# Performance work log

Measured on AMD Instinct MI355X. Metric: run time of the kernel, lower is better.

The kernel has to match this reference:

```python
import math
import jax, jax.numpy as jnp
import numpy as np

NUM_HEADS = 12
NUM_GROUPS = 12
NUM_BUCKETS = 32
MAX_DISTANCE = 128
EPS_GN = 1e-5
EPS_LN = 1e-5


def _layernorm(x, w, b):
    mu = x.mean(axis=-1, keepdims=True)
    xc = x - mu
    inv = jax.lax.rsqrt((xc * xc).mean(axis=-1, keepdims=True) + EPS_LN)
    return xc * inv * w + b


def _rel_pos_bias(T, emb):
    # T5-style bucketed relative position bias -> (1, n_heads, T, T)
    ctx = jnp.arange(T)[:, None]
    mem = jnp.arange(T)[None, :]
    n = -(mem - ctx)  # = context - memory
    nb = NUM_BUCKETS // 2  # bidirectional
    ret = (n < 0).astype(jnp.int32) * nb
    n = jnp.abs(n)
    max_exact = nb // 2
    val_large = max_exact + (
        jnp.log(jnp.maximum(n, 1).astype(jnp.float32) / max_exact)
        / math.log(MAX_DISTANCE / max_exact) * (nb - max_exact)
    ).astype(jnp.int32)
    val_large = jnp.minimum(val_large, nb - 1)
    bucket = ret + jnp.where(n < max_exact, n, val_large)  # (T, T)
    vals = emb[bucket]  # (T, T, He)
    return jnp.transpose(vals, (2, 0, 1))[None]  # (1, He, T, T)


def setup_inputs() -> dict:
    key = jax.random.key(0)
    ks = jax.random.split(key, 12)
    T, B, C, H, W, D = 64, 1, 768, 8, 8, 8
    hd = C // NUM_HEADS
    return {
        "x": jax.random.normal(ks[0], (T, B, C, H, W, D), jnp.float32),
        "norm1_w": jax.random.normal(ks[1], (C,), jnp.float32),
        "w_in": jax.random.normal(ks[2], (3 * C, C), jnp.float32) * 0.02,
        "b_in": jax.random.normal(ks[3], (3 * C,), jnp.float32) * 0.02,
        "qn_w": jax.random.normal(ks[4], (hd,), jnp.float32),
        "qn_b": jnp.zeros((hd,), jnp.float32),
        "kn_w": jax.random.normal(ks[5], (hd,), jnp.float32),
        "kn_b": jnp.zeros((hd,), jnp.float32),
        "rel_emb": jax.random.normal(ks[6], (NUM_BUCKETS, NUM_HEADS), jnp.float32),
        "w_out": jax.random.normal(ks[7], (C, C), jnp.float32) * 0.02,
        "b_out": jax.random.normal(ks[8], (C,), jnp.float32) * 0.02,
        "gamma": jax.random.normal(ks[9], (C,), jnp.float32) * 1e-6,
    }


def reference(x, norm1_w, w_in, b_in, qn_w, qn_b, kn_w, kn_b, rel_emb, w_out, b_out, gamma):
    T, B, C, H, W, D = x.shape
    He = NUM_HEADS
    hd = C // He
    xt = x.reshape(T * B, C, H, W, D)

    # RMSGroupNorm (actually standard group_norm, weight only, no bias)
    xg = xt.reshape(T * B, NUM_GROUPS, C // NUM_GROUPS, H, W, D)
    mu = xg.mean(axis=(2, 3, 4, 5), keepdims=True)
    var = ((xg - mu) ** 2).mean(axis=(2, 3, 4, 5), keepdims=True)
    xn = (xg - mu) * jax.lax.rsqrt(var + EPS_GN)
    xn = xn.reshape(T * B, C, H, W, D) * norm1_w[None, :, None, None, None]

    # 1x1x1 Conv3d input head == per-voxel linear
    qkv = jnp.einsum('ncxyz,oc->noxyz', xn, w_in) + b_in[None, :, None, None, None]

    # rearrange '(t b) (he c) h w d -> (b h w d) he t c'
    qkv = qkv.reshape(T, B, He, 3 * hd, H, W, D)
    qkv = jnp.transpose(qkv, (1, 4, 5, 6, 2, 0, 3)).reshape(B * H * W * D, He, T, 3 * hd)
    q, k, v = jnp.split(qkv, 3, axis=-1)
    q = _layernorm(q, qn_w, qn_b)
    k = _layernorm(k, kn_w, kn_b)

    bias = _rel_pos_bias(T, rel_emb)  # (1, He, T, T)
    scores = jnp.einsum('nhtc,nhsc->nhts', q, k) / math.sqrt(hd) + bias
    att = jax.nn.softmax(scores, axis=-1)
    o = jnp.einsum('nhts,nhsc->nhtc', att, v)  # (BHWD, He, T, hd)

    # rearrange '(b h w d) he t c -> (t b) (he c) h w d'
    o = o.reshape(B, H, W, D, He, T, hd)
    o = jnp.transpose(o, (5, 0, 4, 6, 1, 2, 3)).reshape(T * B, C, H, W, D)

    o = jnp.einsum('ncxyz,oc->noxyz', o, w_out) + b_out[None, :, None, None, None]
    o = o.reshape(T, B, C, H, W, D)

    # layer-scale residual (drop_path = identity)
    return x + gamma[None, None, :, None, None, None] * o
```

## Files before the change

### kernel.cpp

```cpp
#include <hip/hip_runtime.h>


typedef unsigned int u32;
typedef unsigned short u16;
typedef __attribute__((ext_vector_type(4))) float f32x4;
typedef __attribute__((ext_vector_type(8))) short s16x8;

__device__ __forceinline__ float bfl(u32 w){ union{u32 i; float f;} u; u.i = w<<16; return u.f; }
__device__ __forceinline__ float bfh(u32 w){ union{u32 i; float f;} u; u.i = w & 0xffff0000u; return u.f; }
__device__ __forceinline__ u16 f2bf(float f){ union{float ff; u32 i;} u; u.ff = f; u32 r = u.i + 0x7fffu + ((u.i>>16)&1u); return (u16)(r>>16); }
__device__ __forceinline__ u32 pk2(float a, float b){ return (u32)f2bf(a) | ((u32)f2bf(b)<<16); }

__global__ void k_bias(const float* __restrict__ rel, float* __restrict__ bias_d){
  int d = threadIdx.x;
  if (d < 127){
    int delta = d - 63;
    int ret = (delta < 0) ? 16 : 0;
    int a = delta < 0 ? -delta : delta;
    int bkt;
    if (a < 8) bkt = a;
    else {
      float lr = (logf((float)a * 0.125f) / logf(16.0f)) * 8.0f;
      int vl = 8 + (int)lr;
      bkt = vl > 15 ? 15 : vl;
    }
    bkt += ret;
    for (int he = 0; he < 12; ++he) bias_d[he*128 + d] = rel[bkt*12 + he];
  }
}

__global__ void k_cast(const float* __restrict__ a, const float* __restrict__ b,
                       u16* __restrict__ ab, u16* __restrict__ bb){
  const int n1 = 2304*768, n2 = 768*768;
  for (int i = blockIdx.x*blockDim.x + threadIdx.x; i < n1+n2; i += gridDim.x*blockDim.x){
    if (i < n1) ab[i] = f2bf(a[i]);
    else        bb[i-n1] = f2bf(b[i-n1]);
  }
}

__global__ __launch_bounds__(256) void k_stats(const float* __restrict__ x, float* __restrict__ stats){
  __shared__ float red[8];
  const float4* xb = (const float4*)(x + (size_t)blockIdx.x * 32768);
  float s = 0.f, s2 = 0.f;
  for (int i = threadIdx.x; i < 8192; i += 256){
    float4 v = xb[i];
    s  += v.x + v.y + v.z + v.w;
    s2 += v.x*v.x + v.y*v.y + v.z*v.z + v.w*v.w;
  }
  #pragma unroll
  for (int off = 32; off; off >>= 1){ s += __shfl_down(s, off); s2 += __shfl_down(s2, off); }
  int wid = threadIdx.x >> 6;
  if ((threadIdx.x & 63) == 0){ red[wid*2] = s; red[wid*2+1] = s2; }
  __syncthreads();
  if (threadIdx.x == 0){
    float ts = 0.f, ts2 = 0.f;
    for (int w = 0; w < 4; ++w){ ts += red[w*2]; ts2 += red[w*2+1]; }
    float mu  = ts * (1.f/32768.f);
    float var = ts2 * (1.f/32768.f) - mu*mu;
    stats[blockIdx.x*2]   = mu;
    stats[blockIdx.x*2+1] = rsqrtf(var + 1e-5f);
  }
}

__global__ __launch_bounds__(256) void k_norm(const float* __restrict__ x, const float* __restrict__ stats,
                                              const float* __restrict__ w1, u16* __restrict__ xnT){
  __shared__ float ld[64][65];
  const int b = blockIdx.x;
  const int tb = b / 96, rem = b % 96, cb = rem >> 3, vb = rem & 7;
  const float mu  = stats[(tb*12+cb)*2];
  const float inv = stats[(tb*12+cb)*2+1];
  const int tid = threadIdx.x;
  #pragma unroll
  for (int it = 0; it < 4; ++it){
    int chunk = it*256 + tid;
    int cl = chunk >> 4, v4 = chunk & 15;
    float w = w1[cb*64 + cl] * inv;
    float4 v = *(const float4*)(x + ((size_t)(tb*768 + cb*64 + cl)*512 + vb*64 + v4*4));
    ld[cl][v4*4+0] = (v.x - mu) * w;
    ld[cl][v4*4+1] = (v.y - mu) * w;
    ld[cl][v4*4+2] = (v.z - mu) * w;
    ld[cl][v4*4+3] = (v.w - mu) * w;
  }
  __syncthreads();
  #pragma unroll
  for (int it = 0; it < 2; ++it){
    int chunk = it*256 + tid;
    int vl = chunk >> 3, p = chunk & 7;
    u32 ow[4];
    #pragma unroll
    for (int j = 0; j < 4; ++j)
      ow[j] = pk2(ld[p*8 + j*2][vl], ld[p*8 + j*2 + 1][vl]);
    uint4 q4; q4.x = ow[0]; q4.y = ow[1]; q4.z = ow[2]; q4.w = ow[3];
    *(uint4*)(xnT + ((size_t)(tb*512 + vb*64 + vl)*768 + cb*64 + p*8)) = q4;
  }
}

__global__ __launch_bounds__(256) void k_gemm(const u16* __restrict__ At, const u16* __restrict__ Bt,
    const int M, const int K, const int mtiles, const int epi,
    const float* __restrict__ bias, u16* __restrict__ outT,
    const float* __restrict__ xres, const float* __restrict__ gamma,
    const float* __restrict__ bout, float* __restrict__ outp)
{
  __shared__ u16 lta[128*32];
  __shared__ u16 ltb[128*32];
  const int tid = threadIdx.x;
  const int l = tid & 63;
  const int wid = tid >> 6;
  const int wm = wid & 1, wn = wid >> 1;
  const int mt = blockIdx.x % mtiles, nt = blockIdx.x / mtiles;
  const f32x4 z = {0.f, 0.f, 0.f, 0.f};
  f32x4 acc[4][4];
  #pragma unroll
  for (int i = 0; i < 4; ++i)
    #pragma unroll
    for (int j = 0; j < 4; ++j) acc[i][j] = z;
  const int nk = K >> 5;
  const int r0 = tid >> 2, q0 = tid & 3;
  for (int kt = 0; kt < nk; ++kt){
    uint4 av0 = *(const uint4*)(At + (size_t)(mt*128 + r0     )*K + kt*32 + q0*8);
    uint4 bv0 = *(const uint4*)(Bt + (size_t)(nt*128 + r0     )*K + kt*32 + q0*8);
    uint4 av1 = *(const uint4*)(At + (size_t)(mt*128 + r0 + 64)*K + kt*32 + q0*8);
    uint4 bv1 = *(const uint4*)(Bt + (size_t)(nt*128 + r0 + 64)*K + kt*32 + q0*8);
    __syncthreads();
    *(uint4*)&lta[(r0     )*32 + q0*8] = av0;
    *(uint4*)&ltb[(r0     )*32 + q0*8] = bv0;
    *(uint4*)&lta[(r0 + 64)*32 + q0*8] = av1;
    *(uint4*)&ltb[(r0 + 64)*32 + q0*8] = bv1;
    __syncthreads();
    s16x8 fa[4], fb[4];
    #pragma unroll
    for (int f = 0; f < 4; ++f){
      fa[f] = *(const s16x8*)&ltb[(wn*64 + f*16 + (l&15))*32 + ((l>>4)<<3)];
      fb[f] = *(const s16x8*)&lta[(wm*64 + f*16 + (l&15))*32 + ((l>>4)<<3)];
    }
    #pragma unroll
    for (int fn = 0; fn < 4; ++fn)
      #pragma unroll
      for (int fm = 0; fm < 4; ++fm)
        acc[fn][fm] = __builtin_amdgcn_mfma_f32_16x16x32_bf16(fa[fn], fb[fm], acc[fn][fm], 0, 0, 0);
  }
  const int rsub = (l>>4) << 2, cbase = l & 15;
  if (epi == 1){
    #pragma unroll
    for (int fn = 0; fn < 4; ++fn)
      #pragma unroll
      for (int fm = 0; fm < 4; ++fm){
        const int n0 = nt*128 + wn*64 + fn*16 + rsub;
        const int m  = mt*128 + wm*64 + fm*16 + cbase;
        const float bm = bias[m];
        #pragma unroll
        for (int r = 0; r < 4; ++r)
          outT[(size_t)(n0 + r)*M + m] = f2bf(acc[fn][fm][r] + bm);
      }
  } else {
    #pragma unroll
    for (int fn = 0; fn < 4; ++fn)
      #pragma unroll
      for (int fm = 0; fm < 4; ++fm){
        const int n0 = nt*128 + wn*64 + fn*16 + rsub;
        const int m  = mt*128 + wm*64 + fm*16 + cbase;
        const int t = n0 >> 9, vox = n0 & 511;
        const size_t idx = ((size_t)t*768 + m)*512 + vox;
        const float gm = gamma[m], bo = bout[m];
        const float4 xv = *(const float4*)(xres + idx);
        float4 ov;
        ov.x = xv.x + gm*(acc[fn][fm][0] + bo);
        ov.y = xv.y + gm*(acc[fn][fm][1] + bo);
        ov.z = xv.z + gm*(acc[fn][fm][2] + bo);
        ov.w = xv.w + gm*(acc[fn][fm][3] + bo);
        *(float4*)(outp + idx) = ov;
      }
  }
}

__device__ __forceinline__ void ln_row(const uint4* g, const float* __restrict__ w,
                                       const float* __restrict__ b, u16* dst){
  uint4 raw[8];
  #pragma unroll
  for (int i = 0; i < 8; ++i) raw[i] = g[i];
  float s = 0.f, s2 = 0.f;
  #pragma unroll
  for (int i = 0; i < 8; ++i){
    const u32* p = (const u32*)&raw[i];
    #pragma unroll
    for (int j = 0; j < 4; ++j){
      float v0 = bfl(p[j]), v1 = bfh(p[j]);
      s += v0 + v1; s2 += v0*v0 + v1*v1;
    }
  }
  float mu  = s * (1.f/64.f);
  float inv = rsqrtf(s2*(1.f/64.f) - mu*mu + 1e-5f);
  #pragma unroll
  for (int i = 0; i < 8; ++i){
    const u32* p = (const u32*)&raw[i];
    u32 ow[4];
    #pragma unroll
    for (int j = 0; j < 4; ++j){
      int c = i*8 + j*2;
      float v0 = (bfl(p[j]) - mu)*inv*w[c]   + b[c];
      float v1 = (bfh(p[j]) - mu)*inv*w[c+1] + b[c+1];
      ow[j] = pk2(v0, v1);
    }
    uint4 q4; q4.x = ow[0]; q4.y = ow[1]; q4.z = ow[2]; q4.w = ow[3];
    *(uint4*)(dst + i*8) = q4;
  }
}

__global__ __launch_bounds__(64) void k_attn(const u16* __restrict__ qkvT, const float* __restrict__ bias_d,
    const float* __restrict__ qn_w, const float* __restrict__ qn_b,
    const float* __restrict__ kn_w, const float* __restrict__ kn_b,
    u16* __restrict__ oT)
{
  __shared__ u16 qt[64][72], ktl[64][72], vtl[64][72], pt[64][72];
  __shared__ float bd[128];
  const int l = threadIdx.x;
  const int he = blockIdx.x % 12;
  const int vox = blockIdx.x / 12;
  for (int i = l; i < 127; i += 64) bd[i] = bias_d[he*128 + i];
  const size_t rb = ((size_t)(l*512 + vox))*2304 + (size_t)he*192;
  const uint4* g = (const uint4*)(qkvT + rb);
  ln_row(g,     qn_w, qn_b, &qt[l][0]);
  ln_row(g + 8, kn_w, kn_b, &ktl[l][0]);
  #pragma unroll
  for (int i = 0; i < 8; ++i){
    uint4 r = g[16 + i];
    const u32* p = (const u32*)&r;
    #pragma unroll
    for (int j = 0; j < 4; ++j){
      int c = i*8 + j*2;
      vtl[c][l]   = (u16)(p[j] & 0xffffu);
      vtl[c+1][l] = (u16)(p[j] >> 16);
    }
  }
  __syncthreads();
  const f32x4 z = {0.f, 0.f, 0.f, 0.f};
  f32x4 sa[4][4];
  #pragma unroll
  for (int i = 0; i < 4; ++i)
    #pragma unroll
    for (int j = 0; j < 4; ++j) sa[i][j] = z;
  #pragma unroll
  for (int ks = 0; ks < 2; ++ks){
    s16x8 fq[4], fk[4];
    #pragma unroll
    for (int f = 0; f < 4; ++f){
      fq[f] = *(const s16x8*)&qt [f*16 + (l&15)][ks*32 + ((l>>4)<<3)];
      fk[f] = *(const s16x8*)&ktl[f*16 + (l&15)][ks*32 + ((l>>4)<<3)];
    }
    #pragma unroll
    for (int fr = 0; fr < 4; ++fr)
      #pragma unroll
      for (int fc = 0; fc < 4; ++fc)
        sa[fr][fc] = __builtin_amdgcn_mfma_f32_16x16x32_bf16(fq[fr], fk[fc], sa[fr][fc], 0, 0, 0);
  }
  const int cbase = l & 15;
  const int rsub = (l >> 4) << 2;
  #pragma unroll
  for (int fr = 0; fr < 4; ++fr){
    #pragma unroll
    for (int r = 0; r < 4; ++r){
      const int row = fr*16 + rsub + r;
      float v0 = sa[fr][0][r]*0.125f + bd[row - cbase      + 63];
      float v1 = sa[fr][1][r]*0.125f + bd[row - cbase - 16 + 63];
      float v2 = sa[fr][2][r]*0.125f + bd[row - cbase - 32 + 63];
      float v3 = sa[fr][3][r]*0.125f + bd[row - cbase - 48 + 63];
      float m = fmaxf(fmaxf(v0, v1), fmaxf(v2, v3));
      #pragma unroll
      for (int off = 1; off < 16; off <<= 1) m = fmaxf(m, __shfl_xor(m, off));
      v0 = __expf(v0 - m); v1 = __expf(v1 - m); v2 = __expf(v2 - m); v3 = __expf(v3 - m);
      float sum = v0 + v1 + v2 + v3;
      #pragma unroll
      for (int off = 1; off < 16; off <<= 1) sum += __shfl_xor(sum, off);
      float rs = 1.0f / sum;
      pt[row][cbase]      = f2bf(v0*rs);
      pt[row][cbase + 16] = f2bf(v1*rs);
      pt[row][cbase + 32] = f2bf(v2*rs);
      pt[row][cbase + 48] = f2bf(v3*rs);
    }
  }
  __syncthreads();
  f32x4 oa[4][4];
  #pragma unroll
  for (int i = 0; i < 4; ++i)
    #pragma unroll
    for (int j = 0; j < 4; ++j) oa[i][j] = z;
  #pragma unroll
  for (int ks = 0; ks < 2; ++ks){
    s16x8 fp[4], fv[4];
    #pragma unroll
    for (int f = 0; f < 4; ++f){
      fp[f] = *(const s16x8*)&pt [f*16 + (l&15)][ks*32 + ((l>>4)<<3)];
      fv[f] = *(const s16x8*)&vtl[f*16 + (l&15)][ks*32 + ((l>>4)<<3)];
    }
    #pragma unroll
    for (int ft = 0; ft < 4; ++ft)
      #pragma unroll
      for (int fc = 0; fc < 4; ++fc)
        oa[ft][fc] = __builtin_amdgcn_mfma_f32_16x16x32_bf16(fp[ft], fv[fc], oa[ft][fc], 0, 0, 0);
  }
  #pragma unroll
  for (int ft = 0; ft < 4; ++ft)
    #pragma unroll
    for (int fc = 0; fc < 4; ++fc){
      const int t0 = ft*16 + rsub;
      const int c  = fc*16 + cbase;
      #pragma unroll
      for (int r = 0; r < 4; ++r)
        oT[((size_t)((t0 + r)*512 + vox))*768 + he*64 + c] = f2bf(oa[ft][fc][r]);
    }
}

extern "C" void kernel_launch(void* const* d_in, const int* in_sizes, int n_in,
                              void* d_out, int out_size, void* d_ws, size_t ws_size,
                              hipStream_t stream) {
  (void)in_sizes; (void)n_in; (void)out_size; (void)ws_size;
  const float* x      = (const float*)d_in[0];
  const float* norm1w = (const float*)d_in[1];
  const float* w_in   = (const float*)d_in[2];
  const float* b_in   = (const float*)d_in[3];
  const float* qn_w   = (const float*)d_in[4];
  const float* qn_b   = (const float*)d_in[5];
  const float* kn_w   = (const float*)d_in[6];
  const float* kn_b   = (const float*)d_in[7];
  const float* rel    = (const float*)d_in[8];
  const float* w_out  = (const float*)d_in[9];
  const float* b_out  = (const float*)d_in[10];
  const float* gamma  = (const float*)d_in[11];
  float* out = (float*)d_out;

  char* ws = (char*)d_ws;
  float* stats  = (float*)(ws + 0);
  float* bias_d = (float*)(ws + 6144);
  u16*   winb   = (u16*)(ws + 12288);
  u16*   woutb  = (u16*)(ws + 3551232);
  u16*   xnT    = (u16*)(ws + 4730880);
  u16*   oT     = xnT;
  u16*   qkvT   = (u16*)(ws + 55062528);

  k_bias <<<1,    128, 0, stream>>>(rel, bias_d);
  k_cast <<<2048, 256, 0, stream>>>(w_in, w_out, winb, woutb);
  k_stats<<<768,  256, 0, stream>>>(x, stats);
  k_norm <<<6144, 256, 0, stream>>>(x, stats, norm1w, xnT);
  k_gemm <<<4608, 256, 0, stream>>>(winb, xnT, 2304, 768, 18, 1,
                                    b_in, qkvT, nullptr, nullptr, nullptr, nullptr);
  k_attn <<<6144, 64,  0, stream>>>(qkvT, bias_d, qn_w, qn_b, kn_w, kn_b, oT);
  k_gemm <<<1536, 256, 0, stream>>>(woutb, oT, 768, 768, 6, 2,
                                    nullptr, nullptr, x, gamma, b_out, out);
}
```

Measured before the change: 604.7 us.

## Split attention across four waves and use direct global-to-LDS loads in GEMM

The attention kernel now runs 256 threads per block: each wave owns 16 query rows, and the Q/K layernorm is computed cooperatively with 8 lanes per row using shuffles, so global loads are coalesced. The P buffer reuses Q's shared memory, and the second block barrier is replaced by a per-wave LDS waitcnt. Separately, the GEMM tile staging switches to global_load_lds, which writes directly into LDS without passing through registers. These changes aim at better occupancy, memory coalescing and fewer VGPRs. They rely on the LDS layout written by global_load_lds matching the expected 32-element row layout.

```diff
diff --git a/kernel.cpp b/kernel.cpp
--- a/kernel.cpp
+++ b/kernel.cpp
@@ -10,6 +10,11 @@
 __device__ __forceinline__ float bfh(u32 w){ union{u32 i; float f;} u; u.i = w & 0xffff0000u; return u.f; }
 __device__ __forceinline__ u16 f2bf(float f){ union{float ff; u32 i;} u; u.ff = f; u32 r = u.i + 0x7fffu + ((u.i>>16)&1u); return (u16)(r>>16); }
 __device__ __forceinline__ u32 pk2(float a, float b){ return (u32)f2bf(a) | ((u32)f2bf(b)<<16); }
+
+__device__ __forceinline__ void gll16(const u16* g, u16* l){
+  __builtin_amdgcn_global_load_lds((const __attribute__((address_space(1))) void*)g,
+                                   (__attribute__((address_space(3))) void*)l, 16, 0, 0);
+}
 
 __global__ void k_bias(const float* __restrict__ rel, float* __restrict__ bias_d){
   int d = threadIdx.x;
@@ -115,17 +120,19 @@
     #pragma unroll
     for (int j = 0; j < 4; ++j) acc[i][j] = z;
   const int nk = K >> 5;
-  const int r0 = tid >> 2, q0 = tid & 3;
+  const int sr = tid >> 2, sq = tid & 3;
+  const u16* gA = At + (size_t)(mt*128 + sr)*K + sq*8;
+  const u16* gB = Bt + (size_t)(nt*128 + sr)*K + sq*8;
+  u16* lA0 = lta + wid*512;
+  u16* lA1 = lta + 2048 + wid*512;
+  u16* lB0 = ltb + wid*512;
+  u16* lB1 = ltb + 2048 + wid*512;
   for (int kt = 0; kt < nk; ++kt){
-    uint4 av0 = *(const uint4*)(At + (size_t)(mt*128 + r0     )*K + kt*32 + q0*8);
-    uint4 bv0 = *(const uint4*)(Bt + (size_t)(nt*128 + r0     )*K + kt*32 + q0*8);
-    uint4 av1 = *(const uint4*)(At + (size_t)(mt*128 + r0 + 64)*K + kt*32 + q0*8);
-    uint4 bv1 = *(const uint4*)(Bt + (size_t)(nt*128 + r0 + 64)*K + kt*32 + q0*8);
     __syncthreads();
-    *(uint4*)&lta[(r0     )*32 + q0*8] = av0;
-    *(uint4*)&ltb[(r0     )*32 + q0*8] = bv0;
-    *(uint4*)&lta[(r0 + 64)*32 + q0*8] = av1;
-    *(uint4*)&ltb[(r0 + 64)*32 + q0*8] = bv1;
+    gll16(gA + kt*32,              lA0);
+    gll16(gA + kt*32 + (size_t)64*K, lA1);
+    gll16(gB + kt*32,              lB0);
+    gll16(gB + kt*32 + (size_t)64*K, lB1);
     __syncthreads();
     s16x8 fa[4], fb[4];
     #pragma unroll
@@ -173,141 +180,118 @@
   }
 }
 
-__device__ __forceinline__ void ln_row(const uint4* g, const float* __restrict__ w,
-                                       const float* __restrict__ b, u16* dst){
-  uint4 raw[8];
-  #pragma unroll
-  for (int i = 0; i < 8; ++i) raw[i] = g[i];
+__device__ __forceinline__ void ln8(uint4 v, const float* wv, const float* bv, u16* dst){
+  float e[8];
+  const u32* p = (const u32*)&v;
+  #pragma unroll
+  for (int j = 0; j < 4; ++j){ e[2*j] = bfl(p[j]); e[2*j+1] = bfh(p[j]); }
   float s = 0.f, s2 = 0.f;
   #pragma unroll
-  for (int i = 0; i < 8; ++i){
-    const u32* p = (const u32*)&raw[i];
-    #pragma unroll
-    for (int j = 0; j < 4; ++j){
-      float v0 = bfl(p[j]), v1 = bfh(p[j]);
-      s += v0 + v1; s2 += v0*v0 + v1*v1;
-    }
-  }
+  for (int j = 0; j < 8; ++j){ s += e[j]; s2 += e[j]*e[j]; }
+  #pragma unroll
+  for (int off = 1; off < 8; off <<= 1){ s += __shfl_xor(s, off); s2 += __shfl_xor(s2, off); }
   float mu  = s * (1.f/64.f);
   float inv = rsqrtf(s2*(1.f/64.f) - mu*mu + 1e-5f);
-  #pragma unroll
-  for (int i = 0; i < 8; ++i){
-    const u32* p = (const u32*)&raw[i];
-    u32 ow[4];
-    #pragma unroll
-    for (int j = 0; j < 4; ++j){
-      int c = i*8 + j*2;
-      float v0 = (bfl(p[j]) - mu)*inv*w[c]   + b[c];
-      float v1 = (bfh(p[j]) - mu)*inv*w[c+1] + b[c+1];
-      ow[j] = pk2(v0, v1);
-    }
-    uint4 q4; q4.x = ow[0]; q4.y = ow[1]; q4.z = ow[2]; q4.w = ow[3];
-    *(uint4*)(dst + i*8) = q4;
-  }
-}
-
-__global__ __launch_bounds__(64) void k_attn(const u16* __restrict__ qkvT, const float* __restrict__ bias_d,
+  u32 ow[4];
+  #pragma unroll
+  for (int j = 0; j < 4; ++j)
+    ow[j] = pk2((e[2*j]-mu)*inv*wv[2*j] + bv[2*j],
+                (e[2*j+1]-mu)*inv*wv[2*j+1] + bv[2*j+1]);
+  uint4 q4; q4.x = ow[0]; q4.y = ow[1]; q4.z = ow[2]; q4.w = ow[3];
+  *(uint4*)dst = q4;
+}
+
+__global__ __launch_bounds__(256) void k_attn(const u16* __restrict__ qkvT, const float* __restrict__ bias_d,
     const float* __restrict__ qn_w, const float* __restrict__ qn_b,
     const float* __restrict__ kn_w, const float* __restrict__ kn_b,
     u16* __restrict__ oT)
 {
-  __shared__ u16 qt[64][72], ktl[64][72], vtl[64][72], pt[64][72];
+  __shared__ u16 qt[64][72], ktl[64][72], vtl[64][72];
   __shared__ float bd[128];
-  const int l = threadIdx.x;
+  const int tid = threadIdx.x;
+  const int w = tid >> 6, l = tid & 63;
   const int he = blockIdx.x % 12;
   const int vox = blockIdx.x / 12;
-  for (int i = l; i < 127; i += 64) bd[i] = bias_d[he*128 + i];
-  const size_t rb = ((size_t)(l*512 + vox))*2304 + (size_t)he*192;
-  const uint4* g = (const uint4*)(qkvT + rb);
-  ln_row(g,     qn_w, qn_b, &qt[l][0]);
-  ln_row(g + 8, kn_w, kn_b, &ktl[l][0]);
-  #pragma unroll
-  for (int i = 0; i < 8; ++i){
-    uint4 r = g[16 + i];
-    const u32* p = (const u32*)&r;
+  if (tid < 127) bd[tid] = bias_d[he*128 + tid];
+  const int c0 = (l & 7) * 8;
+  const int rl = l >> 3;
+  float qwv[8], qbv[8], kwv[8], kbv[8];
+  *(float4*)&qwv[0] = *(const float4*)(qn_w + c0); *(float4*)&qwv[4] = *(const float4*)(qn_w + c0 + 4);
+  *(float4*)&qbv[0] = *(const float4*)(qn_b + c0); *(float4*)&qbv[4] = *(const float4*)(qn_b + c0 + 4);
+  *(float4*)&kwv[0] = *(const float4*)(kn_w + c0); *(float4*)&kwv[4] = *(const float4*)(kn_w + c0 + 4);
+  *(float4*)&kbv[0] = *(const float4*)(kn_b + c0); *(float4*)&kbv[4] = *(const float4*)(kn_b + c0 + 4);
+  #pragma unroll
+  for (int i = 0; i < 2; ++i){
+    const int r = w*16 + i*8 + rl;
+    const u16* gb = qkvT + ((size_t)(r*512 + vox))*2304 + he*192 + c0;
+    uint4 qv = *(const uint4*)(gb);
+    uint4 kv = *(const uint4*)(gb + 64);
+    uint4 vv = *(const uint4*)(gb + 128);
+    ln8(qv, qwv, qbv, &qt[r][c0]);
+    ln8(kv, kwv, kbv, &ktl[r][c0]);
+    const u32* p = (const u32*)&vv;
     #pragma unroll
     for (int j = 0; j < 4; ++j){
-      int c = i*8 + j*2;
-      vtl[c][l]   = (u16)(p[j] & 0xffffu);
-      vtl[c+1][l] = (u16)(p[j] >> 16);
+      vtl[c0 + 2*j][r]     = (u16)(p[j] & 0xffffu);
+      vtl[c0 + 2*j + 1][r] = (u16)(p[j] >> 16);
     }
   }
   __syncthreads();
+  const int lc = l & 15, lh = l >> 4;
   const f32x4 z = {0.f, 0.f, 0.f, 0.f};
-  f32x4 sa[4][4];
-  #pragma unroll
-  for (int i = 0; i < 4; ++i)
-    #pragma unroll
-    for (int j = 0; j < 4; ++j) sa[i][j] = z;
+  f32x4 sa[4] = {z, z, z, z};
   #pragma unroll
   for (int ks = 0; ks < 2; ++ks){
-    s16x8 fq[4], fk[4];
-    #pragma unroll
-    for (int f = 0; f < 4; ++f){
-      fq[f] = *(const s16x8*)&qt [f*16 + (l&15)][ks*32 + ((l>>4)<<3)];
-      fk[f] = *(const s16x8*)&ktl[f*16 + (l&15)][ks*32 + ((l>>4)<<3)];
-    }
-    #pragma unroll
-    for (int fr = 0; fr < 4; ++fr)
-      #pragma unroll
-      for (int fc = 0; fc < 4; ++fc)
-        sa[fr][fc] = __builtin_amdgcn_mfma_f32_16x16x32_bf16(fq[fr], fk[fc], sa[fr][fc], 0, 0, 0);
-  }
-  const int cbase = l & 15;
-  const int rsub = (l >> 4) << 2;
-  #pragma unroll
-  for (int fr = 0; fr < 4; ++fr){
+    s16x8 fq = *(const s16x8*)&qt[w*16 + lc][ks*32 + lh*8];
+    #pragma unroll
+    for (int fc = 0; fc < 4; ++fc){
+      s16x8 fk = *(const s16x8*)&ktl[fc*16 + lc][ks*32 + lh*8];
+      sa[fc] = __builtin_amdgcn_mfma_f32_16x16x32_bf16(fq, fk, sa[fc], 0, 0, 0);
+    }
+  }
+  u16 (*pt)[72] = qt;
+  const int rsub = lh << 2;
+  #pragma unroll
+  for (int r = 0; r < 4; ++r){
+    const int row = w*16 + rsub + r;
+    float v0 = sa[0][r]*0.125f + bd[row - lc      + 63];
+    float v1 = sa[1][r]*0.125f + bd[row - lc - 16 + 63];
+    float v2 = sa[2][r]*0.125f + bd[row - lc - 32 + 63];
+    float v3 = sa[3][r]*0.125f + bd[row - lc - 48 + 63];
+    float m = fmaxf(fmaxf(v0, v1), fmaxf(v2, v3));
+    #pragma unroll
+    for (int off = 1; off < 16; off <<= 1) m = fmaxf(m, __shfl_xor(m, off));
+    v0 = __expf(v0 - m); v1 = __expf(v1 - m); v2 = __expf(v2 - m); v3 = __expf(v3 - m);
+    float sum = v0 + v1 + v2 + v3;
+    #pragma unroll
+    for (int off = 1; off < 16; off <<= 1) sum += __shfl_xor(sum, off);
+    float rs = 1.0f / sum;
+    pt[row][lc]      = f2bf(v0*rs);
+    pt[row][lc + 16] = f2bf(v1*rs);
+    pt[row][lc + 32] = f2bf(v2*rs);
+    pt[row][lc + 48] = f2bf(v3*rs);
+  }
+  asm volatile("s_waitcnt lgkmcnt(0)" ::: "memory");
+  __builtin_amdgcn_sched_barrier(0);
+  f32x4 oa[4] = {z, z, z, z};
+  #pragma unroll
+  for (int ks = 0; ks < 2; ++ks){
+    s16x8 fp = *(const s16x8*)&pt[w*16 + lc][ks*32 + lh*8];
+    #pragma unroll
+    for (int fc = 0; fc < 4; ++fc){
+      s16x8 fv = *(const s16x8*)&vtl[fc*16 + lc][ks*32 + lh*8];
+      oa[fc] = __builtin_amdgcn_mfma_f32_16x16x32_bf16(fp, fv, oa[fc], 0, 0, 0);
+    }
+  }
+  #pragma unroll
+  for (int fc = 0; fc < 4; ++fc){
+    const int c = fc*16 + lc;
     #pragma unroll
     for (int r = 0; r < 4; ++r){
-      const int row = fr*16 + rsub + r;
-      float v0 = sa[fr][0][r]*0.125f + bd[row - cbase      + 63];
-      float v1 = sa[fr][1][r]*0.125f + bd[row - cbase - 16 + 63];
-      float v2 = sa[fr][2][r]*0.125f + bd[row - cbase - 32 + 63];
-      float v3 = sa[fr][3][r]*0.125f + bd[row - cbase - 48 + 63];
-      float m = fmaxf(fmaxf(v0, v1), fmaxf(v2, v3));
-      #pragma unroll
-      for (int off = 1; off < 16; off <<= 1) m = fmaxf(m, __shfl_xor(m, off));
-      v0 = __expf(v0 - m); v1 = __expf(v1 - m); v2 = __expf(v2 - m); v3 = __expf(v3 - m);
-      float sum = v0 + v1 + v2 + v3;
-      #pragma unroll
-      for (int off = 1; off < 16; off <<= 1) sum += __shfl_xor(sum, off);
-      float rs = 1.0f / sum;
-      pt[row][cbase]      = f2bf(v0*rs);
-      pt[row][cbase + 16] = f2bf(v1*rs);
-      pt[row][cbase + 32] = f2bf(v2*rs);
-      pt[row][cbase + 48] = f2bf(v3*rs);
-    }
-  }
-  __syncthreads();
-  f32x4 oa[4][4];
-  #pragma unroll
-  for (int i = 0; i < 4; ++i)
-    #pragma unroll
-    for (int j = 0; j < 4; ++j) oa[i][j] = z;
-  #pragma unroll
-  for (int ks = 0; ks < 2; ++ks){
-    s16x8 fp[4], fv[4];
-    #pragma unroll
-    for (int f = 0; f < 4; ++f){
-      fp[f] = *(const s16x8*)&pt [f*16 + (l&15)][ks*32 + ((l>>4)<<3)];
-      fv[f] = *(const s16x8*)&vtl[f*16 + (l&15)][ks*32 + ((l>>4)<<3)];
-    }
-    #pragma unroll
-    for (int ft = 0; ft < 4; ++ft)
-      #pragma unroll
-      for (int fc = 0; fc < 4; ++fc)
-        oa[ft][fc] = __builtin_amdgcn_mfma_f32_16x16x32_bf16(fp[ft], fv[fc], oa[ft][fc], 0, 0, 0);
-  }
-  #pragma unroll
-  for (int ft = 0; ft < 4; ++ft)
-    #pragma unroll
-    for (int fc = 0; fc < 4; ++fc){
-      const int t0 = ft*16 + rsub;
-      const int c  = fc*16 + cbase;
-      #pragma unroll
-      for (int r = 0; r < 4; ++r)
-        oT[((size_t)((t0 + r)*512 + vox))*768 + he*64 + c] = f2bf(oa[ft][fc][r]);
-    }
+      const int t = w*16 + rsub + r;
+      oT[((size_t)(t*512 + vox))*768 + he*64 + c] = f2bf(oa[fc][r]);
+    }
+  }
 }
 
 extern "C" void kernel_launch(void* const* d_in, const int* in_sizes, int n_in,
@@ -343,7 +327,7 @@
   k_norm <<<6144, 256, 0, stream>>>(x, stats, norm1w, xnT);
   k_gemm <<<4608, 256, 0, stream>>>(winb, xnT, 2304, 768, 18, 1,
                                     b_in, qkvT, nullptr, nullptr, nullptr, nullptr);
-  k_attn <<<6144, 64,  0, stream>>>(qkvT, bias_d, qn_w, qn_b, kn_w, kn_b, oT);
+  k_attn <<<6144, 256, 0, stream>>>(qkvT, bias_d, qn_w, qn_b, kn_w, kn_b, oT);
   k_gemm <<<1536, 256, 0, stream>>>(woutb, oT, 768, 768, 6, 2,
                                     nullptr, nullptr, x, gamma, b_out, out);
 }
```

New measurement: 574.0 us. 1.05x faster.
